# Performance work log

Hardware: AMD Instinct MI355X
Metric: run time of the kernel (lower is better)

## Reference

```python
import jax, jax.numpy as jnp
import numpy as np

N, E, G = 50000, 300000, 64
VOCAB, EMB, FEAT = 10000, 64, 8
DIN, DH, EDIM = EMB * FEAT, 256, 6


def _lin(k, fout, fin):
    kw, kb = jax.random.split(k)
    w = jax.random.normal(kw, (fout, fin), jnp.float32) / float(np.sqrt(fin))
    b = jax.random.normal(kb, (fout,), jnp.float32) * 0.01
    return w, b


def setup_inputs() -> dict:
    key = jax.random.key(0)
    ks = jax.random.split(key, 10)
    inp = {
        'x_idx': jax.random.randint(ks[0], (N, FEAT), 0, VOCAB),
        'edge_index': jax.random.randint(ks[1], (2, E), 0, N),
        'edge_attr': jax.random.normal(ks[2], (E, EDIM), jnp.float32),
        'batch': jnp.sort(jax.random.randint(ks[3], (N,), 0, G)),
        'emb_table': jax.random.normal(ks[4], (VOCAB, EMB), jnp.float32) * 0.1,
    }
    # two TransformerConv layers: lin_query/key/value (d_in->DH), lin_edge (EDIM->DH), lin_skip (d_in->DH)
    for li, kbase, din in ((1, ks[5], DIN), (2, ks[6], DH)):
        sub = jax.random.split(kbase, 5)
        for j, (wn, bn, fin) in enumerate([('wq', 'bq', din), ('wk', 'bk', din), ('wv', 'bv', din), ('we', 'be', EDIM), ('ws', 'bs', din)]):
            w, b = _lin(sub[j], DH, fin)
            inp['c%d_%s' % (li, wn)] = w
            inp['c%d_%s' % (li, bn)] = b
    for i, (fout, fin, k) in enumerate([(256, 2 * DH, ks[7]), (128, 256, ks[8]), (1, 128, ks[9])]):
        w, b = _lin(k, fout, fin)
        inp['w%d' % (i + 1)] = w
        inp['b%d' % (i + 1)] = b
    return inp


def _tconv(h, src, dst, edge_attr, wq, bq, wk, bk, wv, bv, we, be, ws, bs):
    # PyG TransformerConv, heads=1, concat=True, root_weight=True, beta=False
    n = h.shape[0]
    q = h @ wq.T + bq                      # [N, DH]
    k = h @ wk.T + bk
    v = h @ wv.T + bv
    e = edge_attr @ we.T + be              # [E, DH]
    ke = k[src] + e                        # key fused with edge features
    logits = jnp.sum(q[dst] * ke, axis=-1) / jnp.sqrt(jnp.float32(DH))  # [E]
    m = jax.ops.segment_max(logits, dst, num_segments=n)
    m = jnp.where(jnp.isfinite(m), m, 0.0)
    a = jnp.exp(logits - m[dst])
    s = jax.ops.segment_sum(a, dst, num_segments=n)
    a = a / s[dst]                         # scatter-softmax over incoming edges
    agg = jax.ops.segment_sum((v[src] + e) * a[:, None], dst, num_segments=n)
    return agg + h @ ws.T + bs             # skip connection (root_weight)


def reference(x_idx, edge_index, edge_attr, batch, emb_table,
              c1_wq, c1_bq, c1_wk, c1_bk, c1_wv, c1_bv, c1_we, c1_be, c1_ws, c1_bs,
              c2_wq, c2_bq, c2_wk, c2_bk, c2_wv, c2_bv, c2_we, c2_be, c2_ws, c2_bs,
              w1, b1, w2, b2, w3, b3):
    x = emb_table[x_idx].reshape(x_idx.shape[0], DIN)  # [N, EMB*FEAT]
    src, dst = edge_index[0], edge_index[1]
    h = jax.nn.relu(_tconv(x, src, dst, edge_attr, c1_wq, c1_bq, c1_wk, c1_bk, c1_wv, c1_bv, c1_we, c1_be, c1_ws, c1_bs))
    h = jax.nn.relu(_tconv(h, src, dst, edge_attr, c2_wq, c2_bq, c2_wk, c2_bk, c2_wv, c2_bv, c2_we, c2_be, c2_ws, c2_bs))
    cnt = jax.ops.segment_sum(jnp.ones((h.shape[0],), h.dtype), batch, num_segments=G)
    gap = jax.ops.segment_sum(h, batch, num_segments=G) / jnp.maximum(cnt, 1.0)[:, None]
    gmp = jax.ops.segment_max(h, batch, num_segments=G)
    gmp = jnp.where(jnp.isfinite(gmp), gmp, 0.0)
    r = jnp.concatenate([gap, gmp], axis=1)             # [G, 2*DH]
    o = jax.nn.relu(r @ w1.T + b1)
    o = jax.nn.relu(o @ w2.T + b2)
    # dropout skipped (eval mode)
    return jax.nn.sigmoid(o @ w3.T + b3)[:, 0]          # [G]
```

## Files before the change

kernel.cpp:

```cpp
#include <hip/hip_runtime.h>

typedef unsigned long long ull;
typedef __bf16 bf16x8 __attribute__((ext_vector_type(8)));
typedef float f32x4 __attribute__((ext_vector_type(4)));

__device__ __forceinline__ float bf2f(unsigned short u) {
  union { unsigned int i; float f; } c; c.i = ((unsigned int)u) << 16; return c.f;
}
__device__ __forceinline__ unsigned short f2bf(float f) {
  union { float f; unsigned int i; } c; c.f = f;
  unsigned int u = c.i;
  u += 0x7fffu + ((u >> 16) & 1u);
  return (unsigned short)(u >> 16);
}

__global__ __launch_bounds__(256) void pack_weights(
    const float* __restrict__ wq, const float* __restrict__ wk,
    const float* __restrict__ wv, const float* __restrict__ ws,
    const float* __restrict__ bq, const float* __restrict__ bk,
    const float* __restrict__ bv, const float* __restrict__ bs,
    unsigned short* __restrict__ Wcat, float* __restrict__ bcat, int logK) {
  int idx = blockIdx.x * 256 + threadIdx.x;
  if (idx < 1024) {
    int rr = idx >> 8, cc = idx & 255;
    const float* bp = (rr == 0) ? bq : (rr == 1) ? bk : (rr == 2) ? bv : bs;
    bcat[idx] = bp[cc];
  }
  int K = 1 << logK;
  if (idx >= (1024 << logK)) return;
  int kj = idx & 7;
  int lane = (idx >> 3) & 63;
  int rg = (idx >> 9) & 3;
  int ksbits = logK - 5;
  int ks = (idx >> 11) & ((1 << ksbits) - 1);
  int colt = idx >> (11 + ksbits);
  int quad = lane >> 4, lm = lane & 15;
  int o = colt * 64 + rg * 16 + lm;
  int k = ks * 32 + quad * 8 + kj;
  int rr = o >> 8, oo = o & 255;
  const float* wp = (rr == 0) ? wq : (rr == 1) ? wk : (rr == 2) ? wv : ws;
  Wcat[idx] = f2bf(wp[oo * K + k]);
}

__global__ __launch_bounds__(256) void embed_gather(
    const int* __restrict__ x_idx, const float* __restrict__ emb,
    unsigned short* __restrict__ xbf, int total) {
  int idx = blockIdx.x * 256 + threadIdx.x;
  if (idx >= total) return;
  int n = idx >> 9, d = idx & 511, f = d >> 6, j = d & 63;
  int vi = x_idx[n * 8 + f];
  int n32 = n >> 5, lm = n & 15, half = (n >> 4) & 1;
  int ks = d >> 5, quad = (d >> 3) & 3, kj = d & 7;
  size_t a = (((size_t)(n32 * 16 + ks)) * 2 + half) * 512 + (quad * 16 + lm) * 8 + kj;
  xbf[a] = f2bf(emb[vi * 64 + j]);
}

__global__ __launch_bounds__(256) void count_dst(const int* __restrict__ dst,
                                                 int* __restrict__ counts, int E_) {
  int i = blockIdx.x * 256 + threadIdx.x;
  if (i < E_) atomicAdd(&counts[dst[i]], 1);
}

__global__ __launch_bounds__(256) void alloc_rows(const int* __restrict__ counts,
                                                  int* __restrict__ row_start,
                                                  int* __restrict__ cursor,
                                                  int* __restrict__ total, int n) {
  int i = blockIdx.x * 256 + threadIdx.x;
  int lane = threadIdx.x & 63;
  int c = (i < n) ? counts[i] : 0;
  int incl = c;
#pragma unroll
  for (int off = 1; off < 64; off <<= 1) {
    int t = __shfl_up(incl, off, 64);
    if (lane >= off) incl += t;
  }
  int base = 0;
  if (lane == 63) base = atomicAdd(total, incl);
  base = __shfl(base, 63, 64);
  int st = base + incl - c;
  if (i < n) { row_start[i] = st; cursor[i] = st; }
}

__global__ __launch_bounds__(256) void scatter_edges(
    const int* __restrict__ dst, const int* __restrict__ srcA,
    const float* __restrict__ eattr, int* __restrict__ cursor,
    int* __restrict__ srcs, int* __restrict__ dsts,
    float* __restrict__ ea_perm, int E_) {
  int i = blockIdx.x * 256 + threadIdx.x;
  if (i >= E_) return;
  int d = dst[i];
  int p = atomicAdd(&cursor[d], 1);
  srcs[p] = srcA[i];
  dsts[p] = d;
  const float* ea = eattr + (size_t)i * 6;
  float* eo = ea_perm + (size_t)p * 6;
  eo[0] = ea[0]; eo[1] = ea[1]; eo[2] = ea[2];
  eo[3] = ea[3]; eo[4] = ea[4]; eo[5] = ea[5];
}

template <int K>
__global__ __launch_bounds__(256) void gemm_qkvs(
    const unsigned short* __restrict__ X, const unsigned short* __restrict__ W,
    const float* __restrict__ bcat,
    unsigned short* __restrict__ qout, unsigned short* __restrict__ kout,
    unsigned short* __restrict__ vout, float* __restrict__ sout,
    int Nn, int nrb) {
  __shared__ unsigned short Bs[2][8192];
  const int l = blockIdx.x;
  const int xcd = l & 7, j = l >> 3;
  const int q = nrb >> 3, r = nrb & 7;
  const int cnt = q + (xcd < r ? 1 : 0);
  const int lrb = j >> 4, colt = j & 15;
  if (lrb >= cnt) return;
  const int m_blk = xcd * q + min(xcd, r) + lrb;

  const int tid = threadIdx.x;
  const int wid = tid >> 6;
  const int lane = tid & 63;
  const int quad = lane >> 4, lm = lane & 15;
  const int m_base = m_blk * 128 + wid * 32;
  const int n_base = colt * 64;
  const size_t abase = (size_t)(m_blk * 4 + wid) * (K >> 5) * 1024 + lane * 8;
  const unsigned short* wchunk = W + (size_t)colt * (K >> 5) * 2048;
  const int nc = (K >> 5) / 4;
  f32x4 acc[2][4] = {};

  {
    bf16x8 st0 = *(const bf16x8*)(wchunk + 0 * 2048 + tid * 8);
    bf16x8 st1 = *(const bf16x8*)(wchunk + 1 * 2048 + tid * 8);
    bf16x8 st2 = *(const bf16x8*)(wchunk + 2 * 2048 + tid * 8);
    bf16x8 st3 = *(const bf16x8*)(wchunk + 3 * 2048 + tid * 8);
    *(bf16x8*)(&Bs[0][0 * 2048 + tid * 8]) = st0;
    *(bf16x8*)(&Bs[0][1 * 2048 + tid * 8]) = st1;
    *(bf16x8*)(&Bs[0][2 * 2048 + tid * 8]) = st2;
    *(bf16x8*)(&Bs[0][3 * 2048 + tid * 8]) = st3;
  }
  __syncthreads();

  for (int c = 0; c < nc; c++) {
    bf16x8 st0, st1, st2, st3;
    const bool pf = (c + 1 < nc);
    if (pf) {
      const unsigned short* wp = wchunk + (size_t)(c + 1) * 8192;
      st0 = *(const bf16x8*)(wp + 0 * 2048 + tid * 8);
      st1 = *(const bf16x8*)(wp + 1 * 2048 + tid * 8);
      st2 = *(const bf16x8*)(wp + 2 * 2048 + tid * 8);
      st3 = *(const bf16x8*)(wp + 3 * 2048 + tid * 8);
    }
    const unsigned short* bs = &Bs[c & 1][0];
#pragma unroll
    for (int s = 0; s < 4; s++) {
      const int ks = c * 4 + s;
      const unsigned short* ap = X + abase + (size_t)ks * 1024;
      const unsigned short* bp = bs + s * 2048 + lane * 8;
      bf16x8 a0 = *(const bf16x8*)(ap);
      bf16x8 a1 = *(const bf16x8*)(ap + 512);
      bf16x8 b0 = *(const bf16x8*)(bp);
      bf16x8 b1 = *(const bf16x8*)(bp + 512);
      bf16x8 b2 = *(const bf16x8*)(bp + 1024);
      bf16x8 b3 = *(const bf16x8*)(bp + 1536);
      acc[0][0] = __builtin_amdgcn_mfma_f32_16x16x32_bf16(a0, b0, acc[0][0], 0, 0, 0);
      acc[0][1] = __builtin_amdgcn_mfma_f32_16x16x32_bf16(a0, b1, acc[0][1], 0, 0, 0);
      acc[0][2] = __builtin_amdgcn_mfma_f32_16x16x32_bf16(a0, b2, acc[0][2], 0, 0, 0);
      acc[0][3] = __builtin_amdgcn_mfma_f32_16x16x32_bf16(a0, b3, acc[0][3], 0, 0, 0);
      acc[1][0] = __builtin_amdgcn_mfma_f32_16x16x32_bf16(a1, b0, acc[1][0], 0, 0, 0);
      acc[1][1] = __builtin_amdgcn_mfma_f32_16x16x32_bf16(a1, b1, acc[1][1], 0, 0, 0);
      acc[1][2] = __builtin_amdgcn_mfma_f32_16x16x32_bf16(a1, b2, acc[1][2], 0, 0, 0);
      acc[1][3] = __builtin_amdgcn_mfma_f32_16x16x32_bf16(a1, b3, acc[1][3], 0, 0, 0);
    }
    if (pf) {
      unsigned short* bw = &Bs[(c + 1) & 1][0];
      *(bf16x8*)(bw + 0 * 2048 + tid * 8) = st0;
      *(bf16x8*)(bw + 1 * 2048 + tid * 8) = st1;
      *(bf16x8*)(bw + 2 * 2048 + tid * 8) = st2;
      *(bf16x8*)(bw + 3 * 2048 + tid * 8) = st3;
    }
    __syncthreads();
  }
#pragma unroll
  for (int mi = 0; mi < 2; mi++) {
#pragma unroll
    for (int r2 = 0; r2 < 4; r2++) {
      int row = m_base + mi * 16 + quad * 4 + r2;
      if (row >= Nn) continue;
      size_t rb = (size_t)row * 256;
#pragma unroll
      for (int ni = 0; ni < 4; ni++) {
        int col = n_base + ni * 16 + lm;
        float v = acc[mi][ni][r2] + bcat[col];
        int reg = col >> 8, c2 = col & 255;
        if (reg == 0)       qout[rb + c2] = f2bf(v * 0.0625f);
        else if (reg == 1)  kout[rb + c2] = f2bf(v);
        else if (reg == 2)  vout[rb + c2] = f2bf(v);
        else                sout[rb + c2] = v;
      }
    }
  }
}

__global__ __launch_bounds__(256) void node_prep(
    const unsigned short* __restrict__ qv,
    const float* __restrict__ we, const float* __restrict__ be,
    float* __restrict__ zc, int Nn) {
  __shared__ float we_s[1536];
  __shared__ float be_s[256];
  for (int i = threadIdx.x; i < 1536; i += 256) we_s[i] = we[i];
  be_s[threadIdx.x] = be[threadIdx.x];
  __syncthreads();
  int wid = threadIdx.x >> 6, lane = threadIdx.x & 63;
  int n = blockIdx.x * 4 + wid;
  if (n >= Nn) return;
  int j0 = lane * 4;
  ull uq = *(const ull*)(qv + (size_t)n * 256 + j0);
  float q0 = bf2f((unsigned short)uq), q1 = bf2f((unsigned short)(uq >> 16));
  float q2 = bf2f((unsigned short)(uq >> 32)), q3 = bf2f((unsigned short)(uq >> 48));
  float part[7];
#pragma unroll
  for (int t = 0; t < 6; t++) {
    part[t] = we_s[(j0 + 0) * 6 + t] * q0 + we_s[(j0 + 1) * 6 + t] * q1
            + we_s[(j0 + 2) * 6 + t] * q2 + we_s[(j0 + 3) * 6 + t] * q3;
  }
  part[6] = be_s[j0] * q0 + be_s[j0 + 1] * q1 + be_s[j0 + 2] * q2 + be_s[j0 + 3] * q3;
#pragma unroll
  for (int off = 32; off > 0; off >>= 1) {
#pragma unroll
    for (int t = 0; t < 7; t++) part[t] += __shfl_xor(part[t], off, 64);
  }
  if (lane == 0) {
    float* zp = zc + (size_t)n * 8;
#pragma unroll
    for (int t = 0; t < 7; t++) zp[t] = part[t];
    zp[7] = 0.f;
  }
}

__device__ __forceinline__ float dot4(ull uq, ull uk) {
  return bf2f((unsigned short)uq) * bf2f((unsigned short)uk)
       + bf2f((unsigned short)(uq >> 16)) * bf2f((unsigned short)(uk >> 16))
       + bf2f((unsigned short)(uq >> 32)) * bf2f((unsigned short)(uk >> 32))
       + bf2f((unsigned short)(uq >> 48)) * bf2f((unsigned short)(uk >> 48));
}

#define SEL8_I(a, t) ((t)==0?(a)[0]:(t)==1?(a)[1]:(t)==2?(a)[2]:(t)==3?(a)[3]:(t)==4?(a)[4]:(t)==5?(a)[5]:(t)==6?(a)[6]:(a)[7])

__global__ __launch_bounds__(256) void edge_logits(
    const int* __restrict__ srcs, const int* __restrict__ dsts,
    const float* __restrict__ ea_perm,
    const unsigned short* __restrict__ qv, const unsigned short* __restrict__ kv,
    const float* __restrict__ zc, int E_, float* __restrict__ logits) {
  int wid = threadIdx.x >> 6, lane = threadIdx.x & 63;
  int p0 = (blockIdx.x * 4 + wid) * 8;
  if (p0 >= E_) return;
  int j0 = lane * 4;
  int s_[8], d_[8];
  if (p0 + 8 <= E_) {
    int4 sa = *(const int4*)(srcs + p0), sb = *(const int4*)(srcs + p0 + 4);
    int4 da = *(const int4*)(dsts + p0), db = *(const int4*)(dsts + p0 + 4);
    s_[0] = sa.x; s_[1] = sa.y; s_[2] = sa.z; s_[3] = sa.w;
    s_[4] = sb.x; s_[5] = sb.y; s_[6] = sb.z; s_[7] = sb.w;
    d_[0] = da.x; d_[1] = da.y; d_[2] = da.z; d_[3] = da.w;
    d_[4] = db.x; d_[5] = db.y; d_[6] = db.z; d_[7] = db.w;
  } else {
#pragma unroll
    for (int t = 0; t < 8; t++) {
      int pp = min(p0 + t, E_ - 1);
      s_[t] = srcs[pp]; d_[t] = dsts[pp];
    }
  }
  ull uk[8], uq[8];
#pragma unroll
  for (int t = 0; t < 8; t++) uk[t] = *(const ull*)(kv + (size_t)s_[t] * 256 + j0);
#pragma unroll
  for (int t = 0; t < 8; t++) uq[t] = *(const ull*)(qv + (size_t)d_[t] * 256 + j0);
  float pv[8];
#pragma unroll
  for (int t = 0; t < 8; t++) pv[t] = dot4(uq[t], uk[t]);
#pragma unroll
  for (int off = 32; off > 0; off >>= 1) {
#pragma unroll
    for (int t = 0; t < 8; t++) pv[t] += __shfl_xor(pv[t], off, 64);
  }
  if (lane < 8 && p0 + lane < E_) {
    int t = lane;
    int dd = SEL8_I(d_, t);
    float pvt = SEL8_I(pv, t);
    const float* zp = zc + (size_t)dd * 8;
    const float* u = ea_perm + (size_t)(p0 + t) * 6;
    float zd = zp[0] * u[0] + zp[1] * u[1] + zp[2] * u[2]
             + zp[3] * u[3] + zp[4] * u[4] + zp[5] * u[5] + zp[6];
    logits[p0 + t] = pvt + zd;
  }
}

__global__ __launch_bounds__(256) void node_softmax(
    const int* __restrict__ row_start, const int* __restrict__ counts,
    const float* __restrict__ ea_perm,
    float* __restrict__ logits, float* __restrict__ ubar, int Nn) {
  int wid = threadIdx.x >> 6, lane = threadIdx.x & 63;
  int n = blockIdx.x * 4 + wid;
  if (n >= Nn) return;
  int beg = row_start[n], cnt = counts[n];
  if (cnt == 0) return;
  float lm = -INFINITY;
  for (int b = lane; b < cnt; b += 64) lm = fmaxf(lm, logits[beg + b]);
#pragma unroll
  for (int off = 32; off > 0; off >>= 1) lm = fmaxf(lm, __shfl_xor(lm, off, 64));
  float se = 0.f;
  for (int b = lane; b < cnt; b += 64) se += __expf(logits[beg + b] - lm);
#pragma unroll
  for (int off = 32; off > 0; off >>= 1) se += __shfl_xor(se, off, 64);
  float inv = 1.f / se;
  float u0 = 0.f, u1 = 0.f, u2 = 0.f, u3 = 0.f, u4 = 0.f, u5 = 0.f;
  for (int b = lane; b < cnt; b += 64) {
    int p = beg + b;
    float w = __expf(logits[p] - lm) * inv;
    logits[p] = w;
    const float* up = ea_perm + (size_t)p * 6;
    u0 += w * up[0]; u1 += w * up[1]; u2 += w * up[2];
    u3 += w * up[3]; u4 += w * up[4]; u5 += w * up[5];
  }
#pragma unroll
  for (int off = 32; off > 0; off >>= 1) {
    u0 += __shfl_xor(u0, off, 64); u1 += __shfl_xor(u1, off, 64);
    u2 += __shfl_xor(u2, off, 64); u3 += __shfl_xor(u3, off, 64);
    u4 += __shfl_xor(u4, off, 64); u5 += __shfl_xor(u5, off, 64);
  }
  if (lane == 0) {
    float* up = ubar + (size_t)n * 8;
    up[0] = u0; up[1] = u1; up[2] = u2; up[3] = u3; up[4] = u4; up[5] = u5;
  }
}

#define NPW 8
__global__ __launch_bounds__(256) void edge_agg_final(
    const int* __restrict__ srcs, const int* __restrict__ row_start,
    const int* __restrict__ counts, const float* __restrict__ wgt,
    const unsigned short* __restrict__ vv,
    const float* __restrict__ ubar, const float* __restrict__ skipv,
    const float* __restrict__ we, const float* __restrict__ be,
    int Nn, int mode,
    unsigned short* __restrict__ hout, float* __restrict__ h_acc) {
  __shared__ float we_s[1536];
  __shared__ float be_s[256];
  for (int i = threadIdx.x; i < 1536; i += 256) we_s[i] = we[i];
  be_s[threadIdx.x] = be[threadIdx.x];
  __syncthreads();
  int wave = blockIdx.x * 4 + (threadIdx.x >> 6);
  int lane = threadIdx.x & 63;
  int n0 = wave * NPW;
  if (n0 >= Nn) return;
  int n1 = min(n0 + NPW, Nn);
  int j0 = lane * 4;
  for (int n = n0; n < n1; n++) {
    int cnt = counts[n];
    float a0 = 0.f, a1 = 0.f, a2 = 0.f, a3 = 0.f;
    float e[4] = {0.f, 0.f, 0.f, 0.f};
    if (cnt > 0) {
      int beg = row_start[n];
      for (int i0 = 0; i0 < cnt; i0 += 8) {
        int m = cnt - i0; if (m > 8) m = 8;
        float w8[8];
        int s8[8];
#pragma unroll
        for (int t = 0; t < 8; t++) {
          int pp = beg + i0 + ((t < m) ? t : (m - 1));
          w8[t] = (t < m) ? wgt[pp] : 0.f;
          s8[t] = srcs[pp];
        }
        ull uv[8];
#pragma unroll
        for (int t = 0; t < 8; t++)
          uv[t] = *(const ull*)(vv + (size_t)s8[t] * 256 + j0);
#pragma unroll
        for (int t = 0; t < 8; t++) {
          float ww = w8[t];
          a0 += ww * bf2f((unsigned short)uv[t]);
          a1 += ww * bf2f((unsigned short)(uv[t] >> 16));
          a2 += ww * bf2f((unsigned short)(uv[t] >> 32));
          a3 += ww * bf2f((unsigned short)(uv[t] >> 48));
        }
      }
      float4 u0 = *(const float4*)(ubar + (size_t)n * 8);
      float4 u1 = *(const float4*)(ubar + (size_t)n * 8 + 4);
#pragma unroll
      for (int r = 0; r < 4; r++) {
        int d = j0 + r;
        e[r] = be_s[d]
             + we_s[d * 6 + 0] * u0.x + we_s[d * 6 + 1] * u0.y + we_s[d * 6 + 2] * u0.z
             + we_s[d * 6 + 3] * u0.w + we_s[d * 6 + 4] * u1.x + we_s[d * 6 + 5] * u1.y;
      }
    }
    float4 skv = *(const float4*)(skipv + (size_t)n * 256 + j0);
    float h0 = fmaxf(a0 + e[0] + skv.x, 0.f);
    float h1 = fmaxf(a1 + e[1] + skv.y, 0.f);
    float h2 = fmaxf(a2 + e[2] + skv.z, 0.f);
    float h3 = fmaxf(a3 + e[3] + skv.w, 0.f);
    if (mode == 0) {
      ull hv = (ull)f2bf(h0) | ((ull)f2bf(h1) << 16) | ((ull)f2bf(h2) << 32) | ((ull)f2bf(h3) << 48);
      int n32 = n >> 5, lmn = n & 15, halfn = (n >> 4) & 1;
      int ks = lane >> 3, quadc = (lane >> 1) & 3, kjc = (lane & 1) * 4;
      size_t a = (((size_t)(n32 * 8 + ks)) * 2 + halfn) * 512 + (quadc * 16 + lmn) * 8 + kjc;
      *(ull*)(hout + a) = hv;
    } else {
      float4 o; o.x = h0; o.y = h1; o.z = h2; o.w = h3;
      *(float4*)(h_acc + (size_t)n * 256 + j0) = o;
    }
  }
}

__global__ __launch_bounds__(256) void pool_reduce(
    const float* __restrict__ hfin, const int* __restrict__ batch, int Nn,
    float* __restrict__ gap, unsigned int* __restrict__ gmp) {
  int g = blockIdx.x, s = blockIdx.y, t = threadIdx.x;
  __shared__ int st_s, en_s;
  if (t == 0) {
    int lo = 0, hi = Nn;
    while (lo < hi) { int mid = (lo + hi) >> 1; if (batch[mid] < g) lo = mid + 1; else hi = mid; }
    st_s = lo;
    lo = 0; hi = Nn;
    while (lo < hi) { int mid = (lo + hi) >> 1; if (batch[mid] < g + 1) lo = mid + 1; else hi = mid; }
    en_s = lo;
  }
  __syncthreads();
  int st = st_s, en = en_s;
  int len = en - st;
  if (len <= 0) return;
  int nsplit = gridDim.y;
  int chunk = (len + nsplit - 1) / nsplit;
  int a = st + s * chunk;
  int b = min(a + chunk, en);
  if (a >= b) return;
  float acc = 0.f, mx = 0.f;
  for (int n = a; n < b; n++) {
    float v = hfin[(size_t)n * 256 + t];
    acc += v;
    mx = fmaxf(mx, v);
  }
  atomicAdd(&gap[(size_t)g * 256 + t], acc);
  atomicMax(&gmp[(size_t)g * 256 + t], __float_as_uint(mx));
}

__global__ __launch_bounds__(256) void pool_mlp(
    const float* __restrict__ gap, const unsigned int* __restrict__ gmp,
    const int* __restrict__ batch, int Nn,
    const float* __restrict__ w1, const float* __restrict__ b1,
    const float* __restrict__ w2, const float* __restrict__ b2,
    const float* __restrict__ w3, const float* __restrict__ b3,
    float* __restrict__ out) {
  int g = blockIdx.x, t = threadIdx.x;
  __shared__ float r[512];
  __shared__ float o1[256];
  __shared__ float o2[128];
  __shared__ float red[256];
  __shared__ int cnt_s;
  if (t == 0) {
    int lo = 0, hi = Nn;
    while (lo < hi) { int mid = (lo + hi) >> 1; if (batch[mid] < g) lo = mid + 1; else hi = mid; }
    int st = lo;
    lo = 0; hi = Nn;
    while (lo < hi) { int mid = (lo + hi) >> 1; if (batch[mid] < g + 1) lo = mid + 1; else hi = mid; }
    cnt_s = lo - st;
  }
  __syncthreads();
  float inv = 1.f / fmaxf((float)cnt_s, 1.f);
  r[t] = gap[(size_t)g * 256 + t] * inv;
  r[256 + t] = __uint_as_float(gmp[(size_t)g * 256 + t]);
  __syncthreads();
  {
    float a = b1[t];
    const float* wr = w1 + (size_t)t * 512;
    for (int k = 0; k < 512; k++) a += wr[k] * r[k];
    o1[t] = fmaxf(a, 0.f);
  }
  __syncthreads();
  if (t < 128) {
    float a = b2[t];
    const float* wr = w2 + (size_t)t * 256;
    for (int k = 0; k < 256; k++) a += wr[k] * o1[k];
    o2[t] = fmaxf(a, 0.f);
  }
  __syncthreads();
  red[t] = (t < 128) ? w3[t] * o2[t] : 0.f;
  __syncthreads();
  for (int s = 128; s > 0; s >>= 1) {
    if (t < s) red[t] += red[t + s];
    __syncthreads();
  }
  if (t == 0) out[g] = 1.f / (1.f + expf(-(red[0] + b3[0])));
}

extern "C" void kernel_launch(void* const* d_in, const int* in_sizes, int n_in,
                              void* d_out, int out_size, void* d_ws, size_t ws_size,
                              hipStream_t stream) {
  const int* x_idx      = (const int*)d_in[0];
  const int* edge_index = (const int*)d_in[1];
  const float* eattr    = (const float*)d_in[2];
  const int* batch      = (const int*)d_in[3];
  const float* emb      = (const float*)d_in[4];
  const float* c1_wq = (const float*)d_in[5],  *c1_bq = (const float*)d_in[6];
  const float* c1_wk = (const float*)d_in[7],  *c1_bk = (const float*)d_in[8];
  const float* c1_wv = (const float*)d_in[9],  *c1_bv = (const float*)d_in[10];
  const float* c1_we = (const float*)d_in[11], *c1_be = (const float*)d_in[12];
  const float* c1_ws = (const float*)d_in[13], *c1_bs = (const float*)d_in[14];
  const float* c2_wq = (const float*)d_in[15], *c2_bq = (const float*)d_in[16];
  const float* c2_wk = (const float*)d_in[17], *c2_bk = (const float*)d_in[18];
  const float* c2_wv = (const float*)d_in[19], *c2_bv = (const float*)d_in[20];
  const float* c2_we = (const float*)d_in[21], *c2_be = (const float*)d_in[22];
  const float* c2_ws = (const float*)d_in[23], *c2_bs = (const float*)d_in[24];
  const float* w1 = (const float*)d_in[25], *b1 = (const float*)d_in[26];
  const float* w2 = (const float*)d_in[27], *b2 = (const float*)d_in[28];
  const float* w3 = (const float*)d_in[29], *b3 = (const float*)d_in[30];

  const int Nn = in_sizes[3];
  const int Ee = in_sizes[1] / 2;
  const int nrb = (Nn + 127) / 128;

  char* ws = (char*)d_ws;
  size_t off = 0;
  auto alloc = [&](size_t bytes) -> void* {
    void* p = ws + off;
    off += (bytes + 255) & ~(size_t)255;
    return p;
  };
  unsigned short* xbf   = (unsigned short*)alloc((size_t)nrb * 128 * 512 * 2);
  unsigned short* qbf   = (unsigned short*)alloc((size_t)Nn * 256 * 2);
  unsigned short* kbf   = (unsigned short*)alloc((size_t)Nn * 256 * 2);
  unsigned short* vbf   = (unsigned short*)alloc((size_t)Nn * 256 * 2);
  float*          skipf = (float*)alloc((size_t)Nn * 256 * 4);
  unsigned short* h1bf  = (unsigned short*)alloc((size_t)nrb * 128 * 256 * 2);
  unsigned short* Wcat1 = (unsigned short*)alloc((size_t)1024 * 512 * 2);
  float*          bcat1 = (float*)alloc(1024 * 4);
  unsigned short* Wcat2 = (unsigned short*)alloc((size_t)1024 * 256 * 2);
  float*          bcat2 = (float*)alloc(1024 * 4);
  int*            counts    = (int*)alloc((size_t)Nn * 4);
  int*            row_start = (int*)alloc((size_t)Nn * 4);
  int*            cursor    = (int*)alloc((size_t)Nn * 4);
  int*            srcs      = (int*)alloc((size_t)Ee * 4);
  int*            dsts      = (int*)alloc((size_t)Ee * 4);
  float*          ea_perm   = (float*)alloc((size_t)Ee * 6 * 4);
  float*          logits    = (float*)alloc((size_t)Ee * 4);
  float*          zc        = (float*)alloc((size_t)Nn * 8 * 4);
  float*          ubar      = (float*)alloc((size_t)Nn * 8 * 4);
  int*            total     = (int*)alloc(256);
  float*          gap       = (float*)alloc((size_t)64 * 256 * 4);
  unsigned int*   gmp       = (unsigned int*)alloc((size_t)64 * 256 * 4);
  float* h_acc = (float*)xbf;

  const int* srcA = edge_index;
  const int* dstA = edge_index + Ee;

  hipMemsetAsync(counts, 0, (size_t)Nn * 4, stream);
  hipMemsetAsync(total, 0, 4, stream);
  hipMemsetAsync(gap, 0, (size_t)64 * 256 * 4, stream);
  hipMemsetAsync(gmp, 0, (size_t)64 * 256 * 4, stream);

  pack_weights<<<(1024 * 512 + 255) / 256, 256, 0, stream>>>(
      c1_wq, c1_wk, c1_wv, c1_ws, c1_bq, c1_bk, c1_bv, c1_bs, Wcat1, bcat1, 9);
  pack_weights<<<(1024 * 256 + 255) / 256, 256, 0, stream>>>(
      c2_wq, c2_wk, c2_wv, c2_ws, c2_bq, c2_bk, c2_bv, c2_bs, Wcat2, bcat2, 8);
  embed_gather<<<((Nn * 512) + 255) / 256, 256, 0, stream>>>(x_idx, emb, xbf, Nn * 512);
  count_dst<<<(Ee + 255) / 256, 256, 0, stream>>>(dstA, counts, Ee);
  alloc_rows<<<(Nn + 255) / 256, 256, 0, stream>>>(counts, row_start, cursor, total, Nn);
  scatter_edges<<<(Ee + 255) / 256, 256, 0, stream>>>(dstA, srcA, eattr, cursor,
                                                      srcs, dsts, ea_perm, Ee);

  const int rbmax = nrb / 8 + ((nrb % 8) ? 1 : 0);
  const int ggrid = 8 * rbmax * 16;
  const int egrid = (Ee + 31) / 32;
  const int sgrid = (Nn + NPW * 4 - 1) / (NPW * 4);
  const int ngrid = (Nn + 3) / 4;

  gemm_qkvs<512><<<ggrid, 256, 0, stream>>>(xbf, Wcat1, bcat1, qbf, kbf, vbf,
                                            skipf, Nn, nrb);
  node_prep<<<ngrid, 256, 0, stream>>>(qbf, c1_we, c1_be, zc, Nn);
  edge_logits<<<egrid, 256, 0, stream>>>(srcs, dsts, ea_perm, qbf, kbf, zc, Ee, logits);
  node_softmax<<<ngrid, 256, 0, stream>>>(row_start, counts, ea_perm, logits, ubar, Nn);
  edge_agg_final<<<sgrid, 256, 0, stream>>>(srcs, row_start, counts, logits, vbf,
                                            ubar, skipf, c1_we, c1_be, Nn, 0,
                                            h1bf, nullptr);

  gemm_qkvs<256><<<ggrid, 256, 0, stream>>>(h1bf, Wcat2, bcat2, qbf, kbf, vbf,
                                            skipf, Nn, nrb);
  node_prep<<<ngrid, 256, 0, stream>>>(qbf, c2_we, c2_be, zc, Nn);
  edge_logits<<<egrid, 256, 0, stream>>>(srcs, dsts, ea_perm, qbf, kbf, zc, Ee, logits);
  node_softmax<<<ngrid, 256, 0, stream>>>(row_start, counts, ea_perm, logits, ubar, Nn);
  edge_agg_final<<<sgrid, 256, 0, stream>>>(srcs, row_start, counts, logits, vbf,
                                            ubar, skipf, c2_we, c2_be, Nn, 1,
                                            nullptr, h_acc);

  dim3 pg(64, 16);
  pool_reduce<<<pg, 256, 0, stream>>>(h_acc, batch, Nn, gap, gmp);
  pool_mlp<<<64, 256, 0, stream>>>(gap, gmp, batch, Nn, w1, b1, w2, b2, w3, b3,
                                   (float*)d_out);
}
```

Baseline: 754.8 us.

## Fuse scatter-softmax into aggregation kernel and halve GEMM weight stage size

Removes the separate node_softmax kernel and ubar buffer. The aggregation kernel now computes each node's max and sum-exp, the normalized weights and the weighted edge-attribute mean inline, sharing the weights across lanes via shuffles. This saves a launch and a round trip of logits and ubar through memory per layer. Separately, the QKVS GEMM stages half as many K-slices of weights per shared-memory buffer, which halves LDS use and may raise occupancy, at the cost of more loop iterations and barriers.

```diff
diff --git a/kernel.cpp b/kernel.cpp
--- a/kernel.cpp
+++ b/kernel.cpp
@@ -105,7 +105,7 @@
     unsigned short* __restrict__ qout, unsigned short* __restrict__ kout,
     unsigned short* __restrict__ vout, float* __restrict__ sout,
     int Nn, int nrb) {
-  __shared__ unsigned short Bs[2][8192];
+  __shared__ unsigned short Bs[2][4096];
   const int l = blockIdx.x;
   const int xcd = l & 7, j = l >> 3;
   const int q = nrb >> 3, r = nrb & 7;
@@ -122,35 +122,29 @@
   const int n_base = colt * 64;
   const size_t abase = (size_t)(m_blk * 4 + wid) * (K >> 5) * 1024 + lane * 8;
   const unsigned short* wchunk = W + (size_t)colt * (K >> 5) * 2048;
-  const int nc = (K >> 5) / 4;
+  const int nc = (K >> 5) >> 1;
   f32x4 acc[2][4] = {};
 
   {
     bf16x8 st0 = *(const bf16x8*)(wchunk + 0 * 2048 + tid * 8);
     bf16x8 st1 = *(const bf16x8*)(wchunk + 1 * 2048 + tid * 8);
-    bf16x8 st2 = *(const bf16x8*)(wchunk + 2 * 2048 + tid * 8);
-    bf16x8 st3 = *(const bf16x8*)(wchunk + 3 * 2048 + tid * 8);
     *(bf16x8*)(&Bs[0][0 * 2048 + tid * 8]) = st0;
     *(bf16x8*)(&Bs[0][1 * 2048 + tid * 8]) = st1;
-    *(bf16x8*)(&Bs[0][2 * 2048 + tid * 8]) = st2;
-    *(bf16x8*)(&Bs[0][3 * 2048 + tid * 8]) = st3;
   }
   __syncthreads();
 
   for (int c = 0; c < nc; c++) {
-    bf16x8 st0, st1, st2, st3;
+    bf16x8 st0, st1;
     const bool pf = (c + 1 < nc);
     if (pf) {
-      const unsigned short* wp = wchunk + (size_t)(c + 1) * 8192;
+      const unsigned short* wp = wchunk + (size_t)(c + 1) * 4096;
       st0 = *(const bf16x8*)(wp + 0 * 2048 + tid * 8);
       st1 = *(const bf16x8*)(wp + 1 * 2048 + tid * 8);
-      st2 = *(const bf16x8*)(wp + 2 * 2048 + tid * 8);
-      st3 = *(const bf16x8*)(wp + 3 * 2048 + tid * 8);
     }
     const unsigned short* bs = &Bs[c & 1][0];
 #pragma unroll
-    for (int s = 0; s < 4; s++) {
-      const int ks = c * 4 + s;
+    for (int s = 0; s < 2; s++) {
+      const int ks = c * 2 + s;
       const unsigned short* ap = X + abase + (size_t)ks * 1024;
       const unsigned short* bp = bs + s * 2048 + lane * 8;
       bf16x8 a0 = *(const bf16x8*)(ap);
@@ -172,8 +166,6 @@
       unsigned short* bw = &Bs[(c + 1) & 1][0];
       *(bf16x8*)(bw + 0 * 2048 + tid * 8) = st0;
       *(bf16x8*)(bw + 1 * 2048 + tid * 8) = st1;
-      *(bf16x8*)(bw + 2 * 2048 + tid * 8) = st2;
-      *(bf16x8*)(bw + 3 * 2048 + tid * 8) = st3;
     }
     __syncthreads();
   }
@@ -292,51 +284,12 @@
   }
 }
 
-__global__ __launch_bounds__(256) void node_softmax(
-    const int* __restrict__ row_start, const int* __restrict__ counts,
-    const float* __restrict__ ea_perm,
-    float* __restrict__ logits, float* __restrict__ ubar, int Nn) {
-  int wid = threadIdx.x >> 6, lane = threadIdx.x & 63;
-  int n = blockIdx.x * 4 + wid;
-  if (n >= Nn) return;
-  int beg = row_start[n], cnt = counts[n];
-  if (cnt == 0) return;
-  float lm = -INFINITY;
-  for (int b = lane; b < cnt; b += 64) lm = fmaxf(lm, logits[beg + b]);
-#pragma unroll
-  for (int off = 32; off > 0; off >>= 1) lm = fmaxf(lm, __shfl_xor(lm, off, 64));
-  float se = 0.f;
-  for (int b = lane; b < cnt; b += 64) se += __expf(logits[beg + b] - lm);
-#pragma unroll
-  for (int off = 32; off > 0; off >>= 1) se += __shfl_xor(se, off, 64);
-  float inv = 1.f / se;
-  float u0 = 0.f, u1 = 0.f, u2 = 0.f, u3 = 0.f, u4 = 0.f, u5 = 0.f;
-  for (int b = lane; b < cnt; b += 64) {
-    int p = beg + b;
-    float w = __expf(logits[p] - lm) * inv;
-    logits[p] = w;
-    const float* up = ea_perm + (size_t)p * 6;
-    u0 += w * up[0]; u1 += w * up[1]; u2 += w * up[2];
-    u3 += w * up[3]; u4 += w * up[4]; u5 += w * up[5];
-  }
-#pragma unroll
-  for (int off = 32; off > 0; off >>= 1) {
-    u0 += __shfl_xor(u0, off, 64); u1 += __shfl_xor(u1, off, 64);
-    u2 += __shfl_xor(u2, off, 64); u3 += __shfl_xor(u3, off, 64);
-    u4 += __shfl_xor(u4, off, 64); u5 += __shfl_xor(u5, off, 64);
-  }
-  if (lane == 0) {
-    float* up = ubar + (size_t)n * 8;
-    up[0] = u0; up[1] = u1; up[2] = u2; up[3] = u3; up[4] = u4; up[5] = u5;
-  }
-}
-
 #define NPW 8
-__global__ __launch_bounds__(256) void edge_agg_final(
+__global__ __launch_bounds__(256) void node_agg2(
     const int* __restrict__ srcs, const int* __restrict__ row_start,
-    const int* __restrict__ counts, const float* __restrict__ wgt,
-    const unsigned short* __restrict__ vv,
-    const float* __restrict__ ubar, const float* __restrict__ skipv,
+    const int* __restrict__ counts, const float* __restrict__ logits,
+    const unsigned short* __restrict__ vv, const float* __restrict__ ea_perm,
+    const float* __restrict__ skipv,
     const float* __restrict__ we, const float* __restrict__ be,
     int Nn, int mode,
     unsigned short* __restrict__ hout, float* __restrict__ h_acc) {
@@ -357,14 +310,32 @@
     float e[4] = {0.f, 0.f, 0.f, 0.f};
     if (cnt > 0) {
       int beg = row_start[n];
+      float lmx = -INFINITY;
+      for (int b = lane; b < cnt; b += 64) lmx = fmaxf(lmx, logits[beg + b]);
+#pragma unroll
+      for (int off = 32; off > 0; off >>= 1) lmx = fmaxf(lmx, __shfl_xor(lmx, off, 64));
+      float se = 0.f;
+      for (int b = lane; b < cnt; b += 64) se += __expf(logits[beg + b] - lmx);
+#pragma unroll
+      for (int off = 32; off > 0; off >>= 1) se += __shfl_xor(se, off, 64);
+      float inv = 1.f / se;
+      float ub0 = 0.f, ub1 = 0.f, ub2 = 0.f, ub3 = 0.f, ub4 = 0.f, ub5 = 0.f;
       for (int i0 = 0; i0 < cnt; i0 += 8) {
         int m = cnt - i0; if (m > 8) m = 8;
+        float wlane = 0.f;
+        if (lane < m) {
+          int myp = beg + i0 + lane;
+          wlane = __expf(logits[myp] - lmx) * inv;
+          const float* up = ea_perm + (size_t)myp * 6;
+          ub0 += wlane * up[0]; ub1 += wlane * up[1]; ub2 += wlane * up[2];
+          ub3 += wlane * up[3]; ub4 += wlane * up[4]; ub5 += wlane * up[5];
+        }
         float w8[8];
         int s8[8];
 #pragma unroll
         for (int t = 0; t < 8; t++) {
+          w8[t] = __shfl(wlane, t, 64);
           int pp = beg + i0 + ((t < m) ? t : (m - 1));
-          w8[t] = (t < m) ? wgt[pp] : 0.f;
           s8[t] = srcs[pp];
         }
         ull uv[8];
@@ -380,14 +351,21 @@
           a3 += ww * bf2f((unsigned short)(uv[t] >> 48));
         }
       }
-      float4 u0 = *(const float4*)(ubar + (size_t)n * 8);
-      float4 u1 = *(const float4*)(ubar + (size_t)n * 8 + 4);
+#pragma unroll
+      for (int off = 1; off < 8; off <<= 1) {
+        ub0 += __shfl_xor(ub0, off, 64); ub1 += __shfl_xor(ub1, off, 64);
+        ub2 += __shfl_xor(ub2, off, 64); ub3 += __shfl_xor(ub3, off, 64);
+        ub4 += __shfl_xor(ub4, off, 64); ub5 += __shfl_xor(ub5, off, 64);
+      }
+      ub0 = __shfl(ub0, 0, 64); ub1 = __shfl(ub1, 0, 64);
+      ub2 = __shfl(ub2, 0, 64); ub3 = __shfl(ub3, 0, 64);
+      ub4 = __shfl(ub4, 0, 64); ub5 = __shfl(ub5, 0, 64);
 #pragma unroll
       for (int r = 0; r < 4; r++) {
         int d = j0 + r;
         e[r] = be_s[d]
-             + we_s[d * 6 + 0] * u0.x + we_s[d * 6 + 1] * u0.y + we_s[d * 6 + 2] * u0.z
-             + we_s[d * 6 + 3] * u0.w + we_s[d * 6 + 4] * u1.x + we_s[d * 6 + 5] * u1.y;
+             + we_s[d * 6 + 0] * ub0 + we_s[d * 6 + 1] * ub1 + we_s[d * 6 + 2] * ub2
+             + we_s[d * 6 + 3] * ub3 + we_s[d * 6 + 4] * ub4 + we_s[d * 6 + 5] * ub5;
       }
     }
     float4 skv = *(const float4*)(skipv + (size_t)n * 256 + j0);
@@ -540,7 +518,6 @@
   float*          ea_perm   = (float*)alloc((size_t)Ee * 6 * 4);
   float*          logits    = (float*)alloc((size_t)Ee * 4);
   float*          zc        = (float*)alloc((size_t)Nn * 8 * 4);
-  float*          ubar      = (float*)alloc((size_t)Nn * 8 * 4);
   int*            total     = (int*)alloc(256);
   float*          gap       = (float*)alloc((size_t)64 * 256 * 4);
   unsigned int*   gmp       = (unsigned int*)alloc((size_t)64 * 256 * 4);
@@ -574,19 +551,17 @@
                                             skipf, Nn, nrb);
   node_prep<<<ngrid, 256, 0, stream>>>(qbf, c1_we, c1_be, zc, Nn);
   edge_logits<<<egrid, 256, 0, stream>>>(srcs, dsts, ea_perm, qbf, kbf, zc, Ee, logits);
-  node_softmax<<<ngrid, 256, 0, stream>>>(row_start, counts, ea_perm, logits, ubar, Nn);
-  edge_agg_final<<<sgrid, 256, 0, stream>>>(srcs, row_start, counts, logits, vbf,
-                                            ubar, skipf, c1_we, c1_be, Nn, 0,
-                                            h1bf, nullptr);
+  node_agg2<<<sgrid, 256, 0, stream>>>(srcs, row_start, counts, logits, vbf,
+                                       ea_perm, skipf, c1_we, c1_be, Nn, 0,
+                                       h1bf, nullptr);
 
   gemm_qkvs<256><<<ggrid, 256, 0, stream>>>(h1bf, Wcat2, bcat2, qbf, kbf, vbf,
                                             skipf, Nn, nrb);
   node_prep<<<ngrid, 256, 0, stream>>>(qbf, c2_we, c2_be, zc, Nn);
   edge_logits<<<egrid, 256, 0, stream>>>(srcs, dsts, ea_perm, qbf, kbf, zc, Ee, logits);
-  node_softmax<<<ngrid, 256, 0, stream>>>(row_start, counts, ea_perm, logits, ubar, Nn);
-  edge_agg_final<<<sgrid, 256, 0, stream>>>(srcs, row_start, counts, logits, vbf,
-                                            ubar, skipf, c2_we, c2_be, Nn, 1,
-                                            nullptr, h_acc);
+  node_agg2<<<sgrid, 256, 0, stream>>>(srcs, row_start, counts, logits, vbf,
+                                       ea_perm, skipf, c2_we, c2_be, Nn, 1,
+                                       nullptr, h_acc);
 
   dim3 pg(64, 16);
   pool_reduce<<<pg, 256, 0, stream>>>(h_acc, batch, Nn, gap, gmp);
```

Result: faster. 712.1 us (-5.7%).
